# Kernel optimization log

Hardware: AMD Instinct MI355X
Metric: run time of the kernel (lower is better)

Reference implementation:

```python
import jax, jax.numpy as jnp
import numpy as np

POOLED_H = 7
POOLED_W = 7
SPATIAL_SCALE = 0.25
SAMPLING_RATIO = 2


def setup_inputs() -> dict:
    key = jax.random.key(0)
    k1, k2, k3, k4, k5, k6 = jax.random.split(key, 6)
    B, C, H, W = 2, 256, 200, 272
    N = 1000
    feat = jax.random.normal(k1, (B, C, H, W), dtype=jnp.float32)
    img_h = H / SPATIAL_SCALE  # 800
    img_w = W / SPATIAL_SCALE  # 1088
    bidx = jax.random.randint(k2, (N,), 0, B).astype(jnp.float32)
    x1 = jax.random.uniform(k3, (N,)) * (img_w - 64.0)
    y1 = jax.random.uniform(k4, (N,)) * (img_h - 64.0)
    bw = 16.0 + jax.random.uniform(k5, (N,)) * 200.0
    bh = 16.0 + jax.random.uniform(k6, (N,)) * 200.0
    rois = jnp.stack(
        [bidx, x1, y1, jnp.minimum(x1 + bw, img_w - 1.0), jnp.minimum(y1 + bh, img_h - 1.0)],
        axis=1,
    ).astype(jnp.float32)
    return {"feat": feat, "rois": rois}


def _roi_align(feat, rois):
    """Caffe2-style ROIAlign (aligned=False), avg pooling over sampling grid.
    feat: [B, C, H, W], rois: [N, 5] = [batch_ind, x1, y1, x2, y2] (image coords).
    Returns [N, C, POOLED_H, POOLED_W]."""
    B, C, H, W = feat.shape
    sr = SAMPLING_RATIO
    b = rois[:, 0].astype(jnp.int32)                      # [N]
    sw = rois[:, 1] * SPATIAL_SCALE
    sh = rois[:, 2] * SPATIAL_SCALE
    ew = rois[:, 3] * SPATIAL_SCALE
    eh = rois[:, 4] * SPATIAL_SCALE
    roi_w = jnp.maximum(ew - sw, 1.0)
    roi_h = jnp.maximum(eh - sh, 1.0)
    bin_w = roi_w / POOLED_W
    bin_h = roi_h / POOLED_H
    # Flattened sample coords: idx = ph*sr + i  ->  (idx+0.5)/sr = ph + (i+0.5)/sr
    oy = (jnp.arange(POOLED_H * sr, dtype=jnp.float32) + 0.5) / sr  # [Sy]
    ox = (jnp.arange(POOLED_W * sr, dtype=jnp.float32) + 0.5) / sr  # [Sx]
    ys = sh[:, None] + oy[None, :] * bin_h[:, None]                 # [N, Sy]
    xs = sw[:, None] + ox[None, :] * bin_w[:, None]                 # [N, Sx]
    # Out-of-image samples contribute 0 (CUDA kernel semantics: y < -1 or y > H)
    valid_y = (ys > -1.0) & (ys < H)
    valid_x = (xs > -1.0) & (xs < W)
    # Clamp + corner indices
    yc = jnp.clip(ys, 0.0, H - 1.0)
    xc = jnp.clip(xs, 0.0, W - 1.0)
    yl = jnp.floor(yc).astype(jnp.int32)
    xl = jnp.floor(xc).astype(jnp.int32)
    yh = jnp.minimum(yl + 1, H - 1)
    xh = jnp.minimum(xl + 1, W - 1)
    ly = yc - yl.astype(jnp.float32)   # [N, Sy]
    lx = xc - xl.astype(jnp.float32)   # [N, Sx]
    hy = 1.0 - ly
    hx = 1.0 - lx

    def gather(yi, xi):
        # [N, Sy, Sx, C]
        return feat[b[:, None, None], :, yi[:, :, None], xi[:, None, :]]

    val = (
        (hy[:, :, None] * hx[:, None, :])[..., None] * gather(yl, xl)
        + (hy[:, :, None] * lx[:, None, :])[..., None] * gather(yl, xh)
        + (ly[:, :, None] * hx[:, None, :])[..., None] * gather(yh, xl)
        + (ly[:, :, None] * lx[:, None, :])[..., None] * gather(yh, xh)
    )
    val = val * (valid_y[:, :, None] & valid_x[:, None, :])[..., None]
    N = rois.shape[0]
    # Average sr*sr samples per bin
    val = val.reshape(N, POOLED_H, sr, POOLED_W, sr, C).mean(axis=(2, 4))
    return val.transpose(0, 3, 1, 2)  # [N, C, PH, PW]


def reference(feat, rois):
    return _roi_align(feat, rois)
```

## Files before the change

### kernel.cpp

```cpp
#include <hip/hip_runtime.h>

#define PH 7
#define PW 7
#define SR 2
#define SY (PH * SR)
#define SX (PW * SR)
#define CH 256
#define FH 200
#define FW 272
#define BINS (PH * PW)
#define NPIX (FH * FW)

__device__ __forceinline__ unsigned short f2bf(float f) {
    unsigned x = __float_as_uint(f);
    return (unsigned short)((x + 0x7fffu + ((x >> 16) & 1u)) >> 16);
}
__device__ __forceinline__ float bflo(unsigned u) { return __uint_as_float(u << 16); }
__device__ __forceinline__ float bfhi(unsigned u) { return __uint_as_float(u & 0xffff0000u); }

__global__ __launch_bounds__(256) void transpose_kernel(
    const float* __restrict__ feat, unsigned short* __restrict__ featT) {
    __shared__ unsigned short tile[FW][64];
    const int t  = threadIdx.x;
    const int bh = blockIdx.x;
    const int c0 = blockIdx.y * 64;
    const int b  = bh / FH;
    const int h  = bh % FH;

    const int cl  = t >> 2;
    const int wq0 = t & 3;
    const float* __restrict__ src =
        feat + (size_t)b * CH * NPIX + (size_t)(c0 + cl) * NPIX + (size_t)h * FW;
    #pragma unroll
    for (int k = 0; k < 17; ++k) {
        const int fidx = wq0 + 4 * k;
        const float4 v = *(const float4*)(src + fidx * 4);
        const int w = fidx * 4;
        tile[w + 0][cl] = f2bf(v.x);
        tile[w + 1][cl] = f2bf(v.y);
        tile[w + 2][cl] = f2bf(v.z);
        tile[w + 3][cl] = f2bf(v.w);
    }
    __syncthreads();

    const int cd = t & 31;
    const int wl = t >> 5;
    unsigned* __restrict__ dstu = (unsigned*)featT;
    const size_t pixbase = (size_t)bh * FW;
    #pragma unroll
    for (int k = 0; k < 34; ++k) {
        const int w = wl + 8 * k;
        const unsigned p = *(const unsigned*)&tile[w][2 * cd];
        dstu[(pixbase + w) * (CH / 2) + (c0 >> 1) + cd] = p;
    }
}

__global__ __launch_bounds__(256) void roialign_cl_kernel(
    const unsigned short* __restrict__ featT,
    const float* __restrict__ rois,
    float* __restrict__ out, int N) {
    __shared__ int   s_yl[SY], s_yh[SY];
    __shared__ float s_ly[SY], s_hy[SY];
    __shared__ int   s_xl[SX], s_xh[SX];
    __shared__ float s_lx[SX], s_hx[SX];
    __shared__ unsigned short s_out16[CH * BINS];

    const int n   = blockIdx.x;
    const int tid = threadIdx.x;
    const float* __restrict__ roi = rois + (size_t)n * 5;

    if (tid < SY + SX) {
        const bool isy = (tid < SY);
        const int  idx = isy ? tid : tid - SY;
        const int  lim = isy ? FH : FW;
        const float start = (isy ? roi[2] : roi[1]) * 0.25f;
        const float end_  = (isy ? roi[4] : roi[3]) * 0.25f;
        const float len   = fmaxf(end_ - start, 1.0f);
        const float binsz = len * (isy ? (1.0f / PH) : (1.0f / PW));
        const float s = start + ((float)idx + 0.5f) * (1.0f / SR) * binsz;
        const float valid = (s > -1.0f && s < (float)lim) ? 0.5f : 0.0f;
        const float cc = fminf(fmaxf(s, 0.0f), (float)(lim - 1));
        const int   lo = (int)floorf(cc);
        const int   hi = min(lo + 1, lim - 1);
        const float l  = (cc - (float)lo) * valid;
        const float hw = (1.0f - (cc - (float)lo)) * valid;
        const int   rowstride = FW * (CH / 2);
        if (isy) { s_yl[idx] = lo * rowstride; s_yh[idx] = hi * rowstride;
                   s_ly[idx] = l; s_hy[idx] = hw; }
        else     { s_xl[idx] = lo * (CH / 2);  s_xh[idx] = hi * (CH / 2);
                   s_lx[idx] = l; s_hx[idx] = hw; }
    }
    __syncthreads();

    const int b = (int)roi[0];
    const int q = tid & 63;
    const int g = tid >> 6;
    const unsigned* __restrict__ fbu =
        (const unsigned*)featT + (size_t)b * (FH * FW * (CH / 2)) + q * 2;

    const int bstart = g * 12;
    const int bend   = (g == 3) ? 49 : (g + 1) * 12;

    #pragma unroll 1
    for (int bin = bstart; bin < bend; ++bin) {
        const int ph = bin / 7;
        const int pw = bin - ph * 7;
        const int sy = ph * SR, sx = pw * SR;
        float a0 = 0.f, a1 = 0.f, a2 = 0.f, a3 = 0.f;
        #pragma unroll
        for (int i = 0; i < SR; ++i) {
            const int   yo0 = s_yl[sy + i], yo1 = s_yh[sy + i];
            const float wy1 = s_ly[sy + i], wy0 = s_hy[sy + i];
            #pragma unroll
            for (int j = 0; j < SR; ++j) {
                const int   xo0 = s_xl[sx + j], xo1 = s_xh[sx + j];
                const float wx1 = s_lx[sx + j], wx0 = s_hx[sx + j];
                const uint2 u00 = *(const uint2*)(fbu + yo0 + xo0);
                const uint2 u01 = *(const uint2*)(fbu + yo0 + xo1);
                const uint2 u10 = *(const uint2*)(fbu + yo1 + xo0);
                const uint2 u11 = *(const uint2*)(fbu + yo1 + xo1);
                const float w00 = wy0 * wx0, w01 = wy0 * wx1;
                const float w10 = wy1 * wx0, w11 = wy1 * wx1;
                a0 += w00 * bflo(u00.x) + w01 * bflo(u01.x) + w10 * bflo(u10.x) + w11 * bflo(u11.x);
                a1 += w00 * bfhi(u00.x) + w01 * bfhi(u01.x) + w10 * bfhi(u10.x) + w11 * bfhi(u11.x);
                a2 += w00 * bflo(u00.y) + w01 * bflo(u01.y) + w10 * bflo(u10.y) + w11 * bflo(u11.y);
                a3 += w00 * bfhi(u00.y) + w01 * bfhi(u01.y) + w10 * bfhi(u10.y) + w11 * bfhi(u11.y);
            }
        }
        const int c4 = q * 4;
        s_out16[(c4 + 0) * BINS + bin] = f2bf(a0);
        s_out16[(c4 + 1) * BINS + bin] = f2bf(a1);
        s_out16[(c4 + 2) * BINS + bin] = f2bf(a2);
        s_out16[(c4 + 3) * BINS + bin] = f2bf(a3);
    }
    __syncthreads();

    float* __restrict__ outn = out + (size_t)n * (CH * BINS);
    #pragma unroll
    for (int k = 0; k < BINS; ++k) {
        const int e = k * 256 + tid;
        outn[e] = bflo((unsigned)s_out16[e]);
    }
}

__global__ __launch_bounds__(256) void roialign_kernel(
    const float* __restrict__ feat,
    const float* __restrict__ rois,
    float* __restrict__ out, int N) {
    __shared__ int   s_yl[SY], s_yh[SY];
    __shared__ float s_ly[SY], s_hy[SY];
    __shared__ int   s_xl[SX], s_xh[SX];
    __shared__ float s_lx[SX], s_hx[SX];
    __shared__ float s_out[CH * BINS];

    const int n   = blockIdx.x;
    const int tid = threadIdx.x;
    const float* __restrict__ roi = rois + (size_t)n * 5;

    if (tid < SY + SX) {
        const bool isy = (tid < SY);
        const int  idx = isy ? tid : tid - SY;
        const int  lim = isy ? FH : FW;
        const float start = (isy ? roi[2] : roi[1]) * 0.25f;
        const float end_  = (isy ? roi[4] : roi[3]) * 0.25f;
        const float len   = fmaxf(end_ - start, 1.0f);
        const float binsz = len * (isy ? (1.0f / PH) : (1.0f / PW));
        const float s = start + ((float)idx + 0.5f) * (1.0f / SR) * binsz;
        const float valid = (s > -1.0f && s < (float)lim) ? 1.0f : 0.0f;
        const float cc = fminf(fmaxf(s, 0.0f), (float)(lim - 1));
        const int   lo = (int)floorf(cc);
        const int   hi = min(lo + 1, lim - 1);
        const float l  = (cc - (float)lo) * valid;
        const float hw = (1.0f - (cc - (float)lo)) * valid;
        if (isy) { s_yl[idx] = lo; s_yh[idx] = hi; s_ly[idx] = l; s_hy[idx] = hw; }
        else     { s_xl[idx] = lo; s_xh[idx] = hi; s_lx[idx] = l; s_hx[idx] = hw; }
    }
    __syncthreads();

    const int b = (int)roi[0];
    const int c = tid;
    const float* __restrict__ fp = feat + ((size_t)b * CH + c) * (size_t)NPIX;

    #pragma unroll 1
    for (int ph = 0; ph < PH; ++ph) {
        const int sy0 = ph * SR;
        const float* r00 = fp + s_yl[sy0] * FW;
        const float* r01 = fp + s_yh[sy0] * FW;
        const float* r10 = fp + s_yl[sy0 + 1] * FW;
        const float* r11 = fp + s_yh[sy0 + 1] * FW;
        const float ly0 = s_ly[sy0],     hy0 = s_hy[sy0];
        const float ly1 = s_ly[sy0 + 1], hy1 = s_hy[sy0 + 1];
        for (int pw = 0; pw < PW; ++pw) {
            const int sx0 = pw * SR;
            float acc = 0.0f;
            #pragma unroll
            for (int j = 0; j < SR; ++j) {
                const int   xl = s_xl[sx0 + j], xh = s_xh[sx0 + j];
                const float lx = s_lx[sx0 + j], hx = s_hx[sx0 + j];
                acc += hy0 * (hx * r00[xl] + lx * r00[xh])
                     + ly0 * (hx * r01[xl] + lx * r01[xh]);
                acc += hy1 * (hx * r10[xl] + lx * r10[xh])
                     + ly1 * (hx * r11[xl] + lx * r11[xh]);
            }
            s_out[c * BINS + ph * PW + pw] = acc * 0.25f;
        }
    }
    __syncthreads();

    float* __restrict__ outn = out + (size_t)n * (CH * BINS);
    #pragma unroll
    for (int k = 0; k < BINS; ++k) {
        const int idx = k * 256 + tid;
        outn[idx] = s_out[idx];
    }
}

extern "C" void kernel_launch(void* const* d_in, const int* in_sizes, int n_in,
                              void* d_out, int out_size, void* d_ws, size_t ws_size,
                              hipStream_t stream) {
    const float* feat = (const float*)d_in[0];
    const float* rois = (const float*)d_in[1];
    float* out = (float*)d_out;
    const int N = in_sizes[1] / 5;
    const int B = in_sizes[0] / (CH * NPIX);
    const size_t need = (size_t)B * CH * NPIX * sizeof(unsigned short);

    if (ws_size >= need) {
        unsigned short* featT = (unsigned short*)d_ws;
        dim3 tgrid(B * FH, CH / 64);
        transpose_kernel<<<tgrid, 256, 0, stream>>>(feat, featT);
        roialign_cl_kernel<<<N, 256, 0, stream>>>(featT, rois, out, N);
    } else {
        roialign_kernel<<<N, 256, 0, stream>>>(feat, rois, out, N);
    }
}
```

Measured before the change: 224.4 us.

## Widen ROIAlign gathers to 8 channels per thread with swizzled LDS output

Each thread now handles 8 bf16 channels with 16-byte uint4 gathers instead of 4 channels with uint2, and 8 groups of 32 threads split the 49 bins. The shared output buffer becomes bin-major and XOR-swizzled so each bin's 8 channels go out in one 16-byte LDS store, and the final readout de-swizzles it with a divide by 49. The transpose tile gets padding to reduce bank conflicts. This cuts load-instruction count and LDS stores, at the cost of more integer work in the output loop and fewer threads per bin.

```diff
diff --git a/kernel.cpp b/kernel.cpp
--- a/kernel.cpp
+++ b/kernel.cpp
@@ -20,7 +20,7 @@
 
 __global__ __launch_bounds__(256) void transpose_kernel(
     const float* __restrict__ feat, unsigned short* __restrict__ featT) {
-    __shared__ unsigned short tile[FW][64];
+    __shared__ __align__(16) unsigned short tile[FW][66];
     const int t  = threadIdx.x;
     const int bh = blockIdx.x;
     const int c0 = blockIdx.y * 64;
@@ -63,7 +63,7 @@
     __shared__ float s_ly[SY], s_hy[SY];
     __shared__ int   s_xl[SX], s_xh[SX];
     __shared__ float s_lx[SX], s_hx[SX];
-    __shared__ unsigned short s_out16[CH * BINS];
+    __shared__ __align__(16) unsigned short s_out16[BINS * CH];
 
     const int n   = blockIdx.x;
     const int tid = threadIdx.x;
@@ -92,14 +92,14 @@
     }
     __syncthreads();
 
-    const int b = (int)roi[0];
-    const int q = tid & 63;
-    const int g = tid >> 6;
+    const int b  = (int)roi[0];
+    const int c8 = tid & 31;
+    const int g  = tid >> 5;
     const unsigned* __restrict__ fbu =
-        (const unsigned*)featT + (size_t)b * (FH * FW * (CH / 2)) + q * 2;
-
-    const int bstart = g * 12;
-    const int bend   = (g == 3) ? 49 : (g + 1) * 12;
+        (const unsigned*)featT + (size_t)b * (FH * FW * (CH / 2)) + c8 * 4;
+
+    const int bstart = g * 6;
+    const int bend   = (g == 7) ? BINS : bstart + 6;
 
     #pragma unroll 1
     for (int bin = bstart; bin < bend; ++bin) {
@@ -107,6 +107,7 @@
         const int pw = bin - ph * 7;
         const int sy = ph * SR, sx = pw * SR;
         float a0 = 0.f, a1 = 0.f, a2 = 0.f, a3 = 0.f;
+        float a4 = 0.f, a5 = 0.f, a6 = 0.f, a7 = 0.f;
         #pragma unroll
         for (int i = 0; i < SR; ++i) {
             const int   yo0 = s_yl[sy + i], yo1 = s_yh[sy + i];
@@ -115,31 +116,40 @@
             for (int j = 0; j < SR; ++j) {
                 const int   xo0 = s_xl[sx + j], xo1 = s_xh[sx + j];
                 const float wx1 = s_lx[sx + j], wx0 = s_hx[sx + j];
-                const uint2 u00 = *(const uint2*)(fbu + yo0 + xo0);
-                const uint2 u01 = *(const uint2*)(fbu + yo0 + xo1);
-                const uint2 u10 = *(const uint2*)(fbu + yo1 + xo0);
-                const uint2 u11 = *(const uint2*)(fbu + yo1 + xo1);
+                const uint4 u00 = *(const uint4*)(fbu + yo0 + xo0);
+                const uint4 u01 = *(const uint4*)(fbu + yo0 + xo1);
+                const uint4 u10 = *(const uint4*)(fbu + yo1 + xo0);
+                const uint4 u11 = *(const uint4*)(fbu + yo1 + xo1);
                 const float w00 = wy0 * wx0, w01 = wy0 * wx1;
                 const float w10 = wy1 * wx0, w11 = wy1 * wx1;
                 a0 += w00 * bflo(u00.x) + w01 * bflo(u01.x) + w10 * bflo(u10.x) + w11 * bflo(u11.x);
                 a1 += w00 * bfhi(u00.x) + w01 * bfhi(u01.x) + w10 * bfhi(u10.x) + w11 * bfhi(u11.x);
                 a2 += w00 * bflo(u00.y) + w01 * bflo(u01.y) + w10 * bflo(u10.y) + w11 * bflo(u11.y);
                 a3 += w00 * bfhi(u00.y) + w01 * bfhi(u01.y) + w10 * bfhi(u10.y) + w11 * bfhi(u11.y);
+                a4 += w00 * bflo(u00.z) + w01 * bflo(u01.z) + w10 * bflo(u10.z) + w11 * bflo(u11.z);
+                a5 += w00 * bfhi(u00.z) + w01 * bfhi(u01.z) + w10 * bfhi(u10.z) + w11 * bfhi(u11.z);
+                a6 += w00 * bflo(u00.w) + w01 * bflo(u01.w) + w10 * bflo(u10.w) + w11 * bflo(u11.w);
+                a7 += w00 * bfhi(u00.w) + w01 * bfhi(u01.w) + w10 * bfhi(u10.w) + w11 * bfhi(u11.w);
             }
         }
-        const int c4 = q * 4;
-        s_out16[(c4 + 0) * BINS + bin] = f2bf(a0);
-        s_out16[(c4 + 1) * BINS + bin] = f2bf(a1);
-        s_out16[(c4 + 2) * BINS + bin] = f2bf(a2);
-        s_out16[(c4 + 3) * BINS + bin] = f2bf(a3);
+        uint4 p;
+        p.x = (unsigned)f2bf(a0) | ((unsigned)f2bf(a1) << 16);
+        p.y = (unsigned)f2bf(a2) | ((unsigned)f2bf(a3) << 16);
+        p.z = (unsigned)f2bf(a4) | ((unsigned)f2bf(a5) << 16);
+        p.w = (unsigned)f2bf(a6) | ((unsigned)f2bf(a7) << 16);
+        const int col = (c8 ^ (bin & 31)) * 8;
+        *(uint4*)&s_out16[bin * CH + col] = p;
     }
     __syncthreads();
 
     float* __restrict__ outn = out + (size_t)n * (CH * BINS);
-    #pragma unroll
+    #pragma unroll 1
     for (int k = 0; k < BINS; ++k) {
-        const int e = k * 256 + tid;
-        outn[e] = bflo((unsigned)s_out16[e]);
+        const int e   = k * 256 + tid;
+        const int c   = e / 49;
+        const int bin = e - c * 49;
+        const int oct = (c >> 3) ^ (bin & 31);
+        outn[e] = bflo((unsigned)s_out16[bin * CH + oct * 8 + (c & 7)]);
     }
 }
 
```

After: 226.9 us. About the same (+1.1%).
